# Optimization experiments

Hardware: AMD Instinct MI355X
Metric: run time of the kernel (lower is better)

Reference implementation:

```python
import jax, jax.numpy as jnp
import numpy as np

EPS = 1e-8
ITERS = 3
N, N_IN, D, N_OUT, IN_DIM, OUT_DIM = 256, 128, 256, 32, 64, 64


def squash(x, axis=-1):
    n = jnp.linalg.norm(x, axis=axis, keepdims=True)
    n2 = n * n
    return (n2 / (n2 + 1.0)) * (x / (n + EPS))


def setup_inputs() -> dict:
    key = jax.random.key(0)
    k1, k2, k3 = jax.random.split(key, 3)
    x = jax.random.normal(k1, (N, N_IN, D), dtype=jnp.float32)
    mask = jnp.ones((N, N_IN), dtype=jnp.float32)
    # xavier-uniform-like init scales
    lim_wcap = float(np.sqrt(6.0 / (D + IN_DIM)))
    Wcap = jax.random.uniform(k2, (N_IN, D, IN_DIM), minval=-lim_wcap, maxval=lim_wcap, dtype=jnp.float32)
    Bcap = jnp.zeros((N_IN, IN_DIM), dtype=jnp.float32)
    lim_wv = float(np.sqrt(6.0 / (IN_DIM + OUT_DIM)))
    Wvotes = jax.random.uniform(k3, (N_IN, N_OUT, IN_DIM, OUT_DIM), minval=-lim_wv, maxval=lim_wv, dtype=jnp.float32)
    Bvotes = jnp.zeros((N_IN, N_OUT, 1, OUT_DIM), dtype=jnp.float32)
    return {"x": x, "mask": mask, "Wcap": Wcap, "Bcap": Bcap, "Wvotes": Wvotes, "Bvotes": Bvotes}


def reference(x, mask, Wcap, Bcap, Wvotes, Bvotes):
    n, n_in, _ = x.shape
    n_out = Wvotes.shape[1]
    # per-input-capsule projection D -> in_dim, then squash
    u = squash(jnp.einsum('nid,idh->nih', x, Wcap) + Bcap)        # [N, n_in, in_dim]
    # votes: per (in_caps, out_caps) linear map in_dim -> out_dim
    votes = jnp.einsum('iodh,nid->nioh', Wvotes, u) + Bvotes[:, :, 0, :]  # [N, n_in, n_out, out_dim]
    votes = votes * mask[:, :, None, None]
    ai = jnp.linalg.norm(u, axis=-1)[:, :, None, None]            # [N, n_in, 1, 1]
    bij = jnp.zeros((n, n_in, n_out, 1), dtype=x.dtype)
    leak = jnp.zeros((n, n_in, 1, 1), dtype=x.dtype)
    vj = None
    for it in range(ITERS):
        leaky_bij = jnp.concatenate([leak, bij], axis=2)          # [N, n_in, n_out+1, 1]
        cij = ai * jax.nn.softmax(leaky_bij, axis=2)[:, :, 1:, :]  # [N, n_in, n_out, 1]
        vj = squash(jnp.sum(cij * votes, axis=1))                 # [N, n_out, out_dim]
        if it != ITERS - 1:
            agree = jnp.einsum('nioh,noh->nio', votes, vj)[..., None]
            bij = bij + agree
    return vj
```

## Files before the change

### kernel.cpp

```cpp
#include <hip/hip_runtime.h>

#define NB    256
#define NIN   128
#define DD    256
#define NOUT  32
#define HDIM  64
#define EPS   1e-8f

typedef __attribute__((ext_vector_type(8))) short short8v;
typedef __attribute__((ext_vector_type(4))) float float4v;

__device__ __forceinline__ unsigned short f2bf(float f) {
    unsigned u = __float_as_uint(f);
    u += 0x7fffu + ((u >> 16) & 1u);
    return (unsigned short)(u >> 16);
}
__device__ __forceinline__ float bf2f(unsigned short h) {
    return __uint_as_float(((unsigned)h) << 16);
}

__global__ __launch_bounds__(256, 2) void k_u_ai(
    const float* __restrict__ x, const float* __restrict__ Wcap,
    const float* __restrict__ Bcap, unsigned short* __restrict__ u_hi,
    unsigned short* __restrict__ u_lo, float* __restrict__ ai)
{
    const int i  = blockIdx.x;
    const int n0 = blockIdx.y * 64;
    const int t  = threadIdx.x;

    __shared__ float Wl[128][68];
    __shared__ float xl[64][132];

    const int tn = t >> 4, th = t & 15;
    const int hbase = th * 4;

    float acc[4][4];
    {
        const float4 b = *(const float4*)(Bcap + i * 64 + hbase);
        #pragma unroll
        for (int r = 0; r < 4; ++r) { acc[r][0]=b.x; acc[r][1]=b.y; acc[r][2]=b.z; acc[r][3]=b.w; }
    }

    for (int half = 0; half < 2; ++half) {
        const float4* wsrc = (const float4*)(Wcap + (size_t)i * DD * 64 + (size_t)half * 128 * 64);
        #pragma unroll
        for (int p = 0; p < 8; ++p) {
            int k = t + p * 256;
            float4 v = wsrc[k];
            int d = k >> 4, h4 = (k & 15) * 4;
            *(float4*)&Wl[d][h4] = v;
        }
        #pragma unroll
        for (int p = 0; p < 8; ++p) {
            int k = t + p * 256;
            int row = k >> 5, c4 = (k & 31) * 4;
            float4 v = *(const float4*)(x + ((size_t)(n0 + row) * NIN + i) * DD + half * 128 + c4);
            *(float4*)&xl[row][c4] = v;
        }
        __syncthreads();
        #pragma unroll 4
        for (int d = 0; d < 128; ++d) {
            float a0 = xl[tn*4+0][d], a1 = xl[tn*4+1][d], a2 = xl[tn*4+2][d], a3 = xl[tn*4+3][d];
            float w0 = Wl[d][hbase+0], w1 = Wl[d][hbase+1], w2 = Wl[d][hbase+2], w3 = Wl[d][hbase+3];
            acc[0][0]=fmaf(a0,w0,acc[0][0]); acc[0][1]=fmaf(a0,w1,acc[0][1]); acc[0][2]=fmaf(a0,w2,acc[0][2]); acc[0][3]=fmaf(a0,w3,acc[0][3]);
            acc[1][0]=fmaf(a1,w0,acc[1][0]); acc[1][1]=fmaf(a1,w1,acc[1][1]); acc[1][2]=fmaf(a1,w2,acc[1][2]); acc[1][3]=fmaf(a1,w3,acc[1][3]);
            acc[2][0]=fmaf(a2,w0,acc[2][0]); acc[2][1]=fmaf(a2,w1,acc[2][1]); acc[2][2]=fmaf(a2,w2,acc[2][2]); acc[2][3]=fmaf(a2,w3,acc[2][3]);
            acc[3][0]=fmaf(a3,w0,acc[3][0]); acc[3][1]=fmaf(a3,w1,acc[3][1]); acc[3][2]=fmaf(a3,w2,acc[3][2]); acc[3][3]=fmaf(a3,w3,acc[3][3]);
        }
        __syncthreads();
    }

    #pragma unroll
    for (int r = 0; r < 4; ++r) {
        float s = acc[r][0]*acc[r][0] + acc[r][1]*acc[r][1] + acc[r][2]*acc[r][2] + acc[r][3]*acc[r][3];
        s += __shfl_xor(s, 1); s += __shfl_xor(s, 2); s += __shfl_xor(s, 4); s += __shfl_xor(s, 8);
        float n2 = s, nrm = sqrtf(n2);
        float f = (n2 / (n2 + 1.0f)) / (nrm + EPS);
        int n = n0 + tn * 4 + r;
        float v0 = f*acc[r][0], v1 = f*acc[r][1], v2 = f*acc[r][2], v3 = f*acc[r][3];
        unsigned short ha = f2bf(v0), hb = f2bf(v1), hc = f2bf(v2), hd = f2bf(v3);
        unsigned short la = f2bf(v0 - bf2f(ha)), lb = f2bf(v1 - bf2f(hb));
        unsigned short lc = f2bf(v2 - bf2f(hc)), ld = f2bf(v3 - bf2f(hd));
        size_t eo = ((size_t)n * NIN + i) * HDIM + hbase;
        *(uint2*)(u_hi + eo) = make_uint2((unsigned)ha | ((unsigned)hb << 16), (unsigned)hc | ((unsigned)hd << 16));
        *(uint2*)(u_lo + eo) = make_uint2((unsigned)la | ((unsigned)lb << 16), (unsigned)lc | ((unsigned)ld << 16));
        if (th == 0) ai[(size_t)n * NIN + i] = f * nrm;
    }
}

__global__ __launch_bounds__(256, 4) void k_wconv(
    const float* __restrict__ Wv, unsigned short* __restrict__ Wth,
    unsigned short* __restrict__ Wtl)
{
    const int io = blockIdx.x;
    const int t  = threadIdx.x;
    __shared__ float tile[64][68];

    const float4* src = (const float4*)(Wv + (size_t)io * 4096);
    const int d = t >> 2, hb = (t & 3) * 16;
    #pragma unroll
    for (int q = 0; q < 4; ++q) {
        float4 v = src[t * 4 + q];
        *(float4*)&tile[d][hb + q * 4] = v;
    }
    __syncthreads();
    const int h = t >> 2, d0 = (t & 3) * 16;
    unsigned hp[8], lp[8];
    #pragma unroll
    for (int j = 0; j < 8; ++j) {
        float fa = tile[d0 + 2*j][h], fb = tile[d0 + 2*j + 1][h];
        unsigned short ha = f2bf(fa), hbb = f2bf(fb);
        unsigned short la = f2bf(fa - bf2f(ha)), lb = f2bf(fb - bf2f(hbb));
        hp[j] = (unsigned)ha | ((unsigned)hbb << 16);
        lp[j] = (unsigned)la | ((unsigned)lb << 16);
    }
    size_t eo = (size_t)io * 4096 + (size_t)h * 64 + d0;
    *(uint4*)(Wth + eo)     = make_uint4(hp[0], hp[1], hp[2], hp[3]);
    *(uint4*)(Wth + eo + 8) = make_uint4(hp[4], hp[5], hp[6], hp[7]);
    *(uint4*)(Wtl + eo)     = make_uint4(lp[0], lp[1], lp[2], lp[3]);
    *(uint4*)(Wtl + eo + 8) = make_uint4(lp[4], lp[5], lp[6], lp[7]);
}

__global__ __launch_bounds__(256, 3) void k_votes(
    const unsigned short* __restrict__ u_hi, const unsigned short* __restrict__ u_lo,
    const unsigned short* __restrict__ Wth, const unsigned short* __restrict__ Wtl,
    const float* __restrict__ Bv, const float* __restrict__ mask,
    _Float16* __restrict__ votes, int c0, int cnt)
{
    const int i   = blockIdx.x;
    const int op  = blockIdx.y;
    const int t   = threadIdx.x;
    const int iob = i * 32 + op * 2;

    __shared__ __align__(16) char lds[49920];
    float* biasl = (float*)(lds + 49152);
    float* msk   = (float*)(lds + 49664);

    {
        const int o = t >> 7, cc = t & 127;
        #pragma unroll
        for (int q = 0; q < 4; ++q) {
            int c = cc + q * 128;
            int h = c >> 3, dby = (c & 7) * 16;
            size_t gb = (size_t)(iob + o) * 8192 + (size_t)c * 16;
            uint4 vh = *(const uint4*)((const char*)Wth + gb);
            uint4 vl = *(const uint4*)((const char*)Wtl + gb);
            int lb = o * 16384 + h * 128 + (dby ^ ((h & 7) << 4));
            *(uint4*)(lds + lb)        = vh;
            *(uint4*)(lds + lb + 8192) = vl;
        }
    }
    if (t < 128) biasl[t] = Bv[(size_t)(iob + (t >> 6)) * 64 + (t & 63)];

    const int w = t >> 6, lane = t & 63;
    const int o_l = w & 1, mi0 = (w >> 1) * 2;
    const int lr = lane & 15, lg = lane >> 4;

    const int nzn = (cnt + 63) >> 6;
    for (int nz = 0; nz < nzn; ++nz) {
        const int nbase = nz * 64;
        __syncthreads();
        {
            const int n = t >> 2, s = t & 3;
            bool ok = (nbase + n) < cnt;
            size_t gb = ((size_t)(c0 + nbase + n) * NIN + i) * HDIM * 2;
            #pragma unroll
            for (int p = 0; p < 2; ++p) {
                int dby = s * 32 + p * 16;
                int lb = 32768 + n * 128 + (dby ^ ((n & 7) << 4));
                uint4 vh = ok ? *(const uint4*)((const char*)u_hi + gb + dby) : make_uint4(0,0,0,0);
                uint4 vl = ok ? *(const uint4*)((const char*)u_lo + gb + dby) : make_uint4(0,0,0,0);
                *(uint4*)(lds + lb)        = vh;
                *(uint4*)(lds + lb + 8192) = vl;
            }
        }
        if (t < 64) msk[t] = ((nbase + t) < cnt) ? mask[(size_t)(c0 + nbase + t) * NIN + i] : 0.f;
        __syncthreads();

        float4v acc[2][4];
        #pragma unroll
        for (int a = 0; a < 2; ++a)
            #pragma unroll
            for (int b = 0; b < 4; ++b)
                acc[a][b] = (float4v){0.f, 0.f, 0.f, 0.f};

        #pragma unroll
        for (int ks = 0; ks < 2; ++ks) {
            const int colby = ks * 64 + lg * 16;
            short8v ah[2], al[2], bh[4], bl[4];
            #pragma unroll
            for (int mi = 0; mi < 2; ++mi) {
                int row = (mi0 + mi) * 16 + lr;
                int ob = 32768 + row * 128 + (colby ^ ((row & 7) << 4));
                ah[mi] = *(const short8v*)(lds + ob);
                al[mi] = *(const short8v*)(lds + ob + 8192);
            }
            #pragma unroll
            for (int ni = 0; ni < 4; ++ni) {
                int hrow = ni * 16 + lr;
                int ob = o_l * 16384 + hrow * 128 + (colby ^ ((hrow & 7) << 4));
                bh[ni] = *(const short8v*)(lds + ob);
                bl[ni] = *(const short8v*)(lds + ob + 8192);
            }
            #pragma unroll
            for (int mi = 0; mi < 2; ++mi)
                #pragma unroll
                for (int ni = 0; ni < 4; ++ni) {
                    acc[mi][ni] = __builtin_amdgcn_mfma_f32_16x16x32_bf16(ah[mi], bh[ni], acc[mi][ni], 0, 0, 0);
                    acc[mi][ni] = __builtin_amdgcn_mfma_f32_16x16x32_bf16(al[mi], bh[ni], acc[mi][ni], 0, 0, 0);
                    acc[mi][ni] = __builtin_amdgcn_mfma_f32_16x16x32_bf16(ah[mi], bl[ni], acc[mi][ni], 0, 0, 0);
                }
        }

        #pragma unroll
        for (int mi = 0; mi < 2; ++mi) {
            #pragma unroll
            for (int r = 0; r < 4; ++r) {
                int n_loc = (mi0 + mi) * 16 + lg * 4 + r;
                if (nbase + n_loc < cnt) {
                    float mv = msk[n_loc];
                    size_t sb = ((size_t)(nbase + n_loc) * NIN + i) * 2048;
                    #pragma unroll
                    for (int ni = 0; ni < 4; ++ni) {
                        int h = ni * 16 + lr;
                        float val = (acc[mi][ni][r] + biasl[o_l * 64 + h]) * mv;
                        int q2 = ((ni & 1) << 1) | (lr >> 3);
                        int off = (q2 * 64 + (op * 2 + o_l) * 2 + (ni >> 1)) * 8 + (lr & 7);
                        votes[sb + off] = (_Float16)val;
                    }
                }
            }
        }
    }
}

#define BSLOT(W, LN, J) buf[(W)][((LN) << 5) + (((J) + (LN)) & 31)]

#define LOADSLAB(DST, IDX) do {                                              \
    const uint4* _p = (const uint4*)(vb + (size_t)(IDX) * 2048) + lane;      \
    _Pragma("unroll")                                                        \
    for (int _q = 0; _q < 4; ++_q) {                                         \
        uint4 _v = _p[_q * 64];                                              \
        const _Float16* _h = (const _Float16*)&_v;                           \
        _Pragma("unroll")                                                    \
        for (int _c = 0; _c < 8; ++_c) (DST)[_q*8+_c] = (float)_h[_c];       \
    }                                                                        \
} while (0)

#define RBODY(V, I) do {                                                     \
    const int _i = (I);                                                      \
    float _ag = 0.f;                                                         \
    _Pragma("unroll")                                                        \
    for (int _j = 0; _j < 32; ++_j) _ag = fmaf((V)[_j], vj[_j], _ag);        \
    _ag += __shfl_xor(_ag, 1);                                               \
    float _b = bijl[_i][o] + _ag;                                            \
    if (g == 0) bijl[_i][o] = _b;                                            \
    float _m = _b;                                                           \
    _m = fmaxf(_m, __shfl_xor(_m, 2));  _m = fmaxf(_m, __shfl_xor(_m, 4));   \
    _m = fmaxf(_m, __shfl_xor(_m, 8));  _m = fmaxf(_m, __shfl_xor(_m, 16));  \
    _m = fmaxf(_m, __shfl_xor(_m, 32));                                      \
    _m = fmaxf(_m, 0.f);                                                     \
    float _e = __expf(_b - _m);                                              \
    float _es = _e;                                                          \
    _es += __shfl_xor(_es, 2);  _es += __shfl_xor(_es, 4);                   \
    _es += __shfl_xor(_es, 8);  _es += __shfl_xor(_es, 16);                  \
    _es += __shfl_xor(_es, 32);                                              \
    float _den = _es + __expf(-_m);                                          \
    float _c = ai_s[_i] * _e / _den;                                         \
    _Pragma("unroll")                                                        \
    for (int _j = 0; _j < 32; ++_j) vjp[_j] = fmaf(_c, (V)[_j], vjp[_j]);    \
} while (0)

#define RMERGE(WRITEOUT) do {                                                \
    __syncthreads();                                                         \
    _Pragma("unroll")                                                        \
    for (int _j = 0; _j < 32; ++_j) BSLOT(wv, lane, _j) = vjp[_j];           \
    __syncthreads();                                                         \
    if (wv == 0) {                                                           \
        float _tot[32];                                                      \
        _Pragma("unroll")                                                    \
        for (int _j = 0; _j < 32; ++_j) {                                    \
            float _s = 0.f;                                                  \
            _Pragma("unroll")                                                \
            for (int _w = 0; _w < 16; ++_w) _s += BSLOT(_w, lane, _j);       \
            _tot[_j] = _s; }                                                 \
        float _ss = 0.f;                                                     \
        _Pragma("unroll")                                                    \
        for (int _j = 0; _j < 32; ++_j) _ss = fmaf(_tot[_j], _tot[_j], _ss); \
        _ss += __shfl_xor(_ss, 1);                                           \
        float _nr = sqrtf(_ss);                                              \
        float _f = (_ss / (_ss + 1.0f)) / (_nr + EPS);                       \
        _Pragma("unroll")                                                    \
        for (int _j = 0; _j < 32; ++_j) {                                    \
            float _v = _f * _tot[_j];                                        \
            BSLOT(0, lane, _j) = _v;                                         \
            if (WRITEOUT) out[(size_t)n * 2048 + base + _j] = _v;            \
        }                                                                    \
    }                                                                        \
    __syncthreads();                                                         \
    _Pragma("unroll")                                                        \
    for (int _j = 0; _j < 32; ++_j) vj[_j] = BSLOT(0, lane, _j);             \
} while (0)

__global__ __launch_bounds__(1024) __attribute__((amdgpu_waves_per_eu(4, 4)))
void k_route(
    const _Float16* __restrict__ votes, const float* __restrict__ ai,
    float* __restrict__ out, int n0, int cnt)
{
    const int nl = blockIdx.x;
    const int n  = n0 + nl;
    const int t  = threadIdx.x;
    const int wv = t >> 6;
    const int lane = t & 63;
    const int o = lane >> 1;
    const int g = lane & 1;
    const int base = o * HDIM + g * 32;
    const int ib = wv * 8;

    __shared__ float buf[16][2048];
    __shared__ float bijl[NIN][NOUT + 1];
    __shared__ float ai_s[NIN];

    if (t < NIN) ai_s[t] = ai[(size_t)n * NIN + t];
    for (int idx = t; idx < NIN * (NOUT + 1); idx += 1024) ((float*)bijl)[idx] = 0.f;
    __syncthreads();

    const _Float16* vb = votes + (size_t)nl * (NIN * NOUT * HDIM);

    float s[32], vj[32], vjp[32];

    #pragma unroll
    for (int j = 0; j < 32; ++j) vjp[j] = 0.f;
    #pragma unroll
    for (int k = 0; k < 8; ++k) {
        LOADSLAB(s, ib + k);
        float c = ai_s[ib + k] * (1.0f / 33.0f);
        #pragma unroll
        for (int j = 0; j < 32; ++j) vjp[j] = fmaf(c, s[j], vjp[j]);
    }
    RMERGE(false);

    #pragma unroll
    for (int j = 0; j < 32; ++j) vjp[j] = 0.f;
    #pragma unroll
    for (int k = 0; k < 8; ++k) {
        LOADSLAB(s, ib + k);
        RBODY(s, ib + k);
    }
    RMERGE(false);

    #pragma unroll
    for (int j = 0; j < 32; ++j) vjp[j] = 0.f;
    #pragma unroll
    for (int k = 0; k < 8; ++k) {
        LOADSLAB(s, ib + k);
        RBODY(s, ib + k);
    }
    RMERGE(true);
}

extern "C" void kernel_launch(void* const* d_in, const int* in_sizes, int n_in,
                              void* d_out, int out_size, void* d_ws, size_t ws_size,
                              hipStream_t stream)
{
    const float* x    = (const float*)d_in[0];
    const float* mask = (const float*)d_in[1];
    const float* Wcap = (const float*)d_in[2];
    const float* Bcap = (const float*)d_in[3];
    const float* Wv   = (const float*)d_in[4];
    const float* Bv   = (const float*)d_in[5];
    float* out = (float*)d_out;

    char* ws = (char*)d_ws;
    unsigned short* u_hi = (unsigned short*)ws;
    unsigned short* u_lo = (unsigned short*)(ws + 4194304);
    float*          ai   = (float*)(ws + 8388608);
    unsigned short* Wth  = (unsigned short*)(ws + 8519680);
    unsigned short* Wtl  = (unsigned short*)(ws + 42074112);
    _Float16*       votes= (_Float16*)(ws + 75628544);

    size_t avail = ws_size > 75628544ull ? ws_size - 75628544ull : 0;
    int chunk = 256;
    while (chunk > 4 && (size_t)chunk * 524288ull > avail) chunk >>= 1;

    k_u_ai<<<dim3(NIN, 4), 256, 0, stream>>>(x, Wcap, Bcap, u_hi, u_lo, ai);
    k_wconv<<<NIN * NOUT, 256, 0, stream>>>(Wv, Wth, Wtl);

    for (int cc0 = 0; cc0 < NB; cc0 += chunk) {
        int cnt = (NB - cc0) < chunk ? (NB - cc0) : chunk;
        k_votes<<<dim3(NIN, 16), 256, 0, stream>>>(u_hi, u_lo, Wth, Wtl, Bv, mask, votes, cc0, cnt);
        k_route<<<cnt, 1024, 0, stream>>>(votes, ai, out, cc0, cnt);
    }
}
```

Measured before the change: 698.9 us.

## Split routing into per-pass kernels with atomic reductions across input-capsule chunks

Replaces the single 1024-thread routing kernel (one block per batch item, with LDS reductions across 16 waves) with separate kernels for each routing pass plus a squash kernel. Each pass uses a grid of batch × 4 input-capsule chunks and accumulates partial vj with global float atomics, keeping bij in global memory. The votes chunking loop is also dropped so votes for the whole batch are computed in one launch, which assumes the workspace is large enough. The aim is more parallelism and occupancy than 256 large blocks give. The cost is extra launches, memsets, atomic traffic and rereading votes from global memory on each pass, and the vj/vjp_sum/bij buffers reuse the u_hi/u_lo workspace region after k_votes has consumed it.

After: 1.485 ms. +112.5%, slower.

```diff
diff --git a/kernel.cpp b/kernel.cpp
--- a/kernel.cpp
+++ b/kernel.cpp
@@ -5,6 +5,7 @@
 #define DD    256
 #define NOUT  32
 #define HDIM  64
+#define NV    2048
 #define EPS   1e-8f
 
 typedef __attribute__((ext_vector_type(8))) short short8v;
@@ -125,7 +126,7 @@
     const unsigned short* __restrict__ u_hi, const unsigned short* __restrict__ u_lo,
     const unsigned short* __restrict__ Wth, const unsigned short* __restrict__ Wtl,
     const float* __restrict__ Bv, const float* __restrict__ mask,
-    _Float16* __restrict__ votes, int c0, int cnt)
+    _Float16* __restrict__ votes)
 {
     const int i   = blockIdx.x;
     const int op  = blockIdx.y;
@@ -156,25 +157,23 @@
     const int o_l = w & 1, mi0 = (w >> 1) * 2;
     const int lr = lane & 15, lg = lane >> 4;
 
-    const int nzn = (cnt + 63) >> 6;
-    for (int nz = 0; nz < nzn; ++nz) {
+    for (int nz = 0; nz < 4; ++nz) {
         const int nbase = nz * 64;
         __syncthreads();
         {
             const int n = t >> 2, s = t & 3;
-            bool ok = (nbase + n) < cnt;
-            size_t gb = ((size_t)(c0 + nbase + n) * NIN + i) * HDIM * 2;
+            size_t gb = ((size_t)(nbase + n) * NIN + i) * HDIM * 2;
             #pragma unroll
             for (int p = 0; p < 2; ++p) {
                 int dby = s * 32 + p * 16;
                 int lb = 32768 + n * 128 + (dby ^ ((n & 7) << 4));
-                uint4 vh = ok ? *(const uint4*)((const char*)u_hi + gb + dby) : make_uint4(0,0,0,0);
-                uint4 vl = ok ? *(const uint4*)((const char*)u_lo + gb + dby) : make_uint4(0,0,0,0);
+                uint4 vh = *(const uint4*)((const char*)u_hi + gb + dby);
+                uint4 vl = *(const uint4*)((const char*)u_lo + gb + dby);
                 *(uint4*)(lds + lb)        = vh;
                 *(uint4*)(lds + lb + 8192) = vl;
             }
         }
-        if (t < 64) msk[t] = ((nbase + t) < cnt) ? mask[(size_t)(c0 + nbase + t) * NIN + i] : 0.f;
+        if (t < 64) msk[t] = mask[(size_t)(nbase + t) * NIN + i];
         __syncthreads();
 
         float4v acc[2][4];
@@ -217,27 +216,23 @@
             #pragma unroll
             for (int r = 0; r < 4; ++r) {
                 int n_loc = (mi0 + mi) * 16 + lg * 4 + r;
-                if (nbase + n_loc < cnt) {
-                    float mv = msk[n_loc];
-                    size_t sb = ((size_t)(nbase + n_loc) * NIN + i) * 2048;
-                    #pragma unroll
-                    for (int ni = 0; ni < 4; ++ni) {
-                        int h = ni * 16 + lr;
-                        float val = (acc[mi][ni][r] + biasl[o_l * 64 + h]) * mv;
-                        int q2 = ((ni & 1) << 1) | (lr >> 3);
-                        int off = (q2 * 64 + (op * 2 + o_l) * 2 + (ni >> 1)) * 8 + (lr & 7);
-                        votes[sb + off] = (_Float16)val;
-                    }
+                float mv = msk[n_loc];
+                size_t sb = ((size_t)(nbase + n_loc) * NIN + i) * NV;
+                #pragma unroll
+                for (int ni = 0; ni < 4; ++ni) {
+                    int h = ni * 16 + lr;
+                    float val = (acc[mi][ni][r] + biasl[o_l * 64 + h]) * mv;
+                    int q2 = ((ni & 1) << 1) | (lr >> 3);
+                    int off = (q2 * 64 + (op * 2 + o_l) * 2 + (ni >> 1)) * 8 + (lr & 7);
+                    votes[sb + off] = (_Float16)val;
                 }
             }
         }
     }
 }
 
-#define BSLOT(W, LN, J) buf[(W)][((LN) << 5) + (((J) + (LN)) & 31)]
-
-#define LOADSLAB(DST, IDX) do {                                              \
-    const uint4* _p = (const uint4*)(vb + (size_t)(IDX) * 2048) + lane;      \
+#define LOADS16(DST, N, I) do {                                              \
+    const uint4* _p = (const uint4*)(votes + ((size_t)(N) * NIN + (I)) * NV) + lane; \
     _Pragma("unroll")                                                        \
     for (int _q = 0; _q < 4; ++_q) {                                         \
         uint4 _v = _p[_q * 64];                                              \
@@ -247,116 +242,112 @@
     }                                                                        \
 } while (0)
 
-#define RBODY(V, I) do {                                                     \
-    const int _i = (I);                                                      \
-    float _ag = 0.f;                                                         \
-    _Pragma("unroll")                                                        \
-    for (int _j = 0; _j < 32; ++_j) _ag = fmaf((V)[_j], vj[_j], _ag);        \
-    _ag += __shfl_xor(_ag, 1);                                               \
-    float _b = bijl[_i][o] + _ag;                                            \
-    if (g == 0) bijl[_i][o] = _b;                                            \
-    float _m = _b;                                                           \
-    _m = fmaxf(_m, __shfl_xor(_m, 2));  _m = fmaxf(_m, __shfl_xor(_m, 4));   \
-    _m = fmaxf(_m, __shfl_xor(_m, 8));  _m = fmaxf(_m, __shfl_xor(_m, 16));  \
-    _m = fmaxf(_m, __shfl_xor(_m, 32));                                      \
-    _m = fmaxf(_m, 0.f);                                                     \
-    float _e = __expf(_b - _m);                                              \
-    float _es = _e;                                                          \
-    _es += __shfl_xor(_es, 2);  _es += __shfl_xor(_es, 4);                   \
-    _es += __shfl_xor(_es, 8);  _es += __shfl_xor(_es, 16);                  \
-    _es += __shfl_xor(_es, 32);                                              \
-    float _den = _es + __expf(-_m);                                          \
-    float _c = ai_s[_i] * _e / _den;                                         \
-    _Pragma("unroll")                                                        \
-    for (int _j = 0; _j < 32; ++_j) vjp[_j] = fmaf(_c, (V)[_j], vjp[_j]);    \
-} while (0)
-
-#define RMERGE(WRITEOUT) do {                                                \
-    __syncthreads();                                                         \
-    _Pragma("unroll")                                                        \
-    for (int _j = 0; _j < 32; ++_j) BSLOT(wv, lane, _j) = vjp[_j];           \
-    __syncthreads();                                                         \
-    if (wv == 0) {                                                           \
-        float _tot[32];                                                      \
-        _Pragma("unroll")                                                    \
-        for (int _j = 0; _j < 32; ++_j) {                                    \
-            float _s = 0.f;                                                  \
-            _Pragma("unroll")                                                \
-            for (int _w = 0; _w < 16; ++_w) _s += BSLOT(_w, lane, _j);       \
-            _tot[_j] = _s; }                                                 \
-        float _ss = 0.f;                                                     \
-        _Pragma("unroll")                                                    \
-        for (int _j = 0; _j < 32; ++_j) _ss = fmaf(_tot[_j], _tot[_j], _ss); \
-        _ss += __shfl_xor(_ss, 1);                                           \
-        float _nr = sqrtf(_ss);                                              \
-        float _f = (_ss / (_ss + 1.0f)) / (_nr + EPS);                       \
-        _Pragma("unroll")                                                    \
-        for (int _j = 0; _j < 32; ++_j) {                                    \
-            float _v = _f * _tot[_j];                                        \
-            BSLOT(0, lane, _j) = _v;                                         \
-            if (WRITEOUT) out[(size_t)n * 2048 + base + _j] = _v;            \
-        }                                                                    \
-    }                                                                        \
-    __syncthreads();                                                         \
-    _Pragma("unroll")                                                        \
-    for (int _j = 0; _j < 32; ++_j) vj[_j] = BSLOT(0, lane, _j);             \
-} while (0)
-
-__global__ __launch_bounds__(1024) __attribute__((amdgpu_waves_per_eu(4, 4)))
-void k_route(
+__global__ __launch_bounds__(256) void k_p1(
     const _Float16* __restrict__ votes, const float* __restrict__ ai,
-    float* __restrict__ out, int n0, int cnt)
-{
-    const int nl = blockIdx.x;
-    const int n  = n0 + nl;
-    const int t  = threadIdx.x;
-    const int wv = t >> 6;
-    const int lane = t & 63;
-    const int o = lane >> 1;
-    const int g = lane & 1;
-    const int base = o * HDIM + g * 32;
-    const int ib = wv * 8;
-
-    __shared__ float buf[16][2048];
-    __shared__ float bijl[NIN][NOUT + 1];
-    __shared__ float ai_s[NIN];
-
-    if (t < NIN) ai_s[t] = ai[(size_t)n * NIN + t];
-    for (int idx = t; idx < NIN * (NOUT + 1); idx += 1024) ((float*)bijl)[idx] = 0.f;
-    __syncthreads();
-
-    const _Float16* vb = votes + (size_t)nl * (NIN * NOUT * HDIM);
-
-    float s[32], vj[32], vjp[32];
-
+    float* __restrict__ vjp_sum)
+{
+    const int n = blockIdx.x, ic = blockIdx.y;
+    const int t = threadIdx.x;
+    const int w = t >> 6, lane = t & 63;
+    const int o = lane >> 1, g = lane & 1;
+    const int ib = ic * 32 + w * 8;
+
+    float vjp[32];
     #pragma unroll
     for (int j = 0; j < 32; ++j) vjp[j] = 0.f;
-    #pragma unroll
+
     for (int k = 0; k < 8; ++k) {
-        LOADSLAB(s, ib + k);
-        float c = ai_s[ib + k] * (1.0f / 33.0f);
+        const int i = ib + k;
+        float c = ai[(size_t)n * NIN + i] * (1.0f / 33.0f);
+        const uint4* p = (const uint4*)(votes + ((size_t)n * NIN + i) * NV) + lane;
+        #pragma unroll
+        for (int q = 0; q < 4; ++q) {
+            uint4 v = p[q * 64];
+            const _Float16* h = (const _Float16*)&v;
+            #pragma unroll
+            for (int cc = 0; cc < 8; ++cc) vjp[q*8+cc] = fmaf(c, (float)h[cc], vjp[q*8+cc]);
+        }
+    }
+    float* dst = vjp_sum + (size_t)n * NV + o * 64 + g * 32;
+    #pragma unroll
+    for (int j = 0; j < 32; ++j) atomicAdd(dst + j, vjp[j]);
+}
+
+__global__ __launch_bounds__(256) void k_p23(
+    const _Float16* __restrict__ votes, const float* __restrict__ ai,
+    const float* __restrict__ vj_in, float* __restrict__ bij,
+    float* __restrict__ vjp_sum, int final_pass)
+{
+    const int n = blockIdx.x, ic = blockIdx.y;
+    const int t = threadIdx.x;
+    const int w = t >> 6, lane = t & 63;
+    const int o = lane >> 1, g = lane & 1;
+    const int ib = ic * 32 + w * 8;
+
+    float vjr[32];
+    {
+        const float4* vp = (const float4*)(vj_in + (size_t)n * NV + o * 64 + g * 32);
+        #pragma unroll
+        for (int q = 0; q < 8; ++q) {
+            float4 v = vp[q];
+            vjr[q*4+0]=v.x; vjr[q*4+1]=v.y; vjr[q*4+2]=v.z; vjr[q*4+3]=v.w;
+        }
+    }
+
+    float vjp[32];
+    #pragma unroll
+    for (int j = 0; j < 32; ++j) vjp[j] = 0.f;
+
+    for (int k = 0; k < 8; ++k) {
+        const int i = ib + k;
+        float s[32];
+        LOADS16(s, n, i);
+
+        float ag = 0.f;
+        #pragma unroll
+        for (int j = 0; j < 32; ++j) ag = fmaf(s[j], vjr[j], ag);
+        ag += __shfl_xor(ag, 1);
+
+        size_t bo = ((size_t)n * NIN + i) * NOUT + o;
+        float b = bij[bo] + ag;
+        if (!final_pass && g == 0) bij[bo] = b;
+
+        float m = b;
+        m = fmaxf(m, __shfl_xor(m, 2));  m = fmaxf(m, __shfl_xor(m, 4));
+        m = fmaxf(m, __shfl_xor(m, 8));  m = fmaxf(m, __shfl_xor(m, 16));
+        m = fmaxf(m, __shfl_xor(m, 32));
+        m = fmaxf(m, 0.f);
+        float e = __expf(b - m);
+        float es = e;
+        es += __shfl_xor(es, 2);  es += __shfl_xor(es, 4);
+        es += __shfl_xor(es, 8);  es += __shfl_xor(es, 16);
+        es += __shfl_xor(es, 32);
+        float den = es + __expf(-m);
+        float c = ai[(size_t)n * NIN + i] * e / den;
+
         #pragma unroll
         for (int j = 0; j < 32; ++j) vjp[j] = fmaf(c, s[j], vjp[j]);
     }
-    RMERGE(false);
-
-    #pragma unroll
-    for (int j = 0; j < 32; ++j) vjp[j] = 0.f;
-    #pragma unroll
-    for (int k = 0; k < 8; ++k) {
-        LOADSLAB(s, ib + k);
-        RBODY(s, ib + k);
-    }
-    RMERGE(false);
-
-    #pragma unroll
-    for (int j = 0; j < 32; ++j) vjp[j] = 0.f;
-    #pragma unroll
-    for (int k = 0; k < 8; ++k) {
-        LOADSLAB(s, ib + k);
-        RBODY(s, ib + k);
-    }
-    RMERGE(true);
+
+    float* dst = vjp_sum + (size_t)n * NV + o * 64 + g * 32;
+    #pragma unroll
+    for (int j = 0; j < 32; ++j) atomicAdd(dst + j, vjp[j]);
+}
+
+__global__ __launch_bounds__(256) void k_sq(
+    float* __restrict__ vjp_sum, float* __restrict__ dst, int zero)
+{
+    const int row  = blockIdx.x * 4 + (threadIdx.x >> 6);
+    const int lane = threadIdx.x & 63;
+    size_t idx = (size_t)row * 64 + lane;
+    float v = vjp_sum[idx];
+    float ss = v * v;
+    ss += __shfl_xor(ss, 1);  ss += __shfl_xor(ss, 2);  ss += __shfl_xor(ss, 4);
+    ss += __shfl_xor(ss, 8);  ss += __shfl_xor(ss, 16); ss += __shfl_xor(ss, 32);
+    float nr = sqrtf(ss);
+    float f = (ss / (ss + 1.0f)) / (nr + EPS);
+    dst[idx] = f * v;
+    if (zero) vjp_sum[idx] = 0.f;
 }
 
 extern "C" void kernel_launch(void* const* d_in, const int* in_sizes, int n_in,
@@ -379,16 +370,22 @@
     unsigned short* Wtl  = (unsigned short*)(ws + 42074112);
     _Float16*       votes= (_Float16*)(ws + 75628544);
 
-    size_t avail = ws_size > 75628544ull ? ws_size - 75628544ull : 0;
-    int chunk = 256;
-    while (chunk > 4 && (size_t)chunk * 524288ull > avail) chunk >>= 1;
+    float* vj      = (float*)ws;
+    float* vjp_sum = (float*)(ws + 2097152);
+    float* bij     = (float*)(ws + 4194304);
 
     k_u_ai<<<dim3(NIN, 4), 256, 0, stream>>>(x, Wcap, Bcap, u_hi, u_lo, ai);
     k_wconv<<<NIN * NOUT, 256, 0, stream>>>(Wv, Wth, Wtl);
-
-    for (int cc0 = 0; cc0 < NB; cc0 += chunk) {
-        int cnt = (NB - cc0) < chunk ? (NB - cc0) : chunk;
-        k_votes<<<dim3(NIN, 16), 256, 0, stream>>>(u_hi, u_lo, Wth, Wtl, Bv, mask, votes, cc0, cnt);
-        k_route<<<cnt, 1024, 0, stream>>>(votes, ai, out, cc0, cnt);
-    }
-}
+    k_votes<<<dim3(NIN, 16), 256, 0, stream>>>(u_hi, u_lo, Wth, Wtl, Bv, mask, votes);
+
+    hipMemsetAsync(vjp_sum, 0, (size_t)NB * NV * 4, stream);
+    hipMemsetAsync(bij,     0, (size_t)NB * NIN * NOUT * 4, stream);
+
+    dim3 gp(NB, 4);
+    k_p1 <<<gp, 256, 0, stream>>>(votes, ai, vjp_sum);
+    k_sq <<<(NB * NOUT) / 4, 256, 0, stream>>>(vjp_sum, vj, 1);
+    k_p23<<<gp, 256, 0, stream>>>(votes, ai, vj, bij, vjp_sum, 0);
+    k_sq <<<(NB * NOUT) / 4, 256, 0, stream>>>(vjp_sum, vj, 1);
+    k_p23<<<gp, 256, 0, stream>>>(votes, ai, vj, bij, vjp_sum, 1);
+    k_sq <<<(NB * NOUT) / 4, 256, 0, stream>>>(vjp_sum, out, 0);
+}
```
